# Kernel optimization log

Measured on AMD Instinct MI355X. Metric: run time of the kernel, lower is better.

## Reference

```python
import jax, jax.numpy as jnp
import numpy as np

KEEP_RATIO = 0.5
TEMPERATURE = 1.0
MIN_GATE = 0.0
EPS = 1e-06


def setup_inputs() -> dict:
    key = jax.random.key(0)
    k1, k2 = jax.random.split(key)
    B, C = 8192, 4096
    token = jax.random.normal(k1, (B, C), dtype=jnp.float32)
    proxy = jax.random.normal(k2, (B, C), dtype=jnp.float32)
    return {"token": token, "proxy": proxy}


def reference(token, proxy):
    tok = token  # [B, C]
    px = jax.lax.stop_gradient(proxy)  # detach_proxy=True
    score = jnp.abs(tok * px)  # [B, C]
    B, C = score.shape
    k = max(1, int(round(C * KEEP_RATIO)))
    # hard mask: top-k indices per row -> scatter 1.0
    _, topk_idx = jax.lax.top_k(score, k)  # [B, k]
    rows = jnp.arange(B)[:, None]
    hard_mask = jnp.zeros_like(score).at[rows, topk_idx].set(1.0)
    # per-row standardization (torch.std is unbiased -> ddof=1)
    mu = jnp.mean(score, axis=-1, keepdims=True)
    sigma = jnp.maximum(jnp.std(score, axis=-1, ddof=1, keepdims=True), EPS)
    z = (score - mu) / sigma / max(TEMPERATURE, EPS)
    soft_gate = jax.nn.sigmoid(z)
    if MIN_GATE > 0:
        soft_gate = soft_gate * (1.0 - MIN_GATE) + MIN_GATE
    gate = soft_gate * (1.0 - hard_mask) + hard_mask
    return tok * gate
```

## Files before the change

### kernel.cpp

```cpp
#include <hip/hip_runtime.h>
#include <math.h>

#define CLS   4096
#define KSEL  2048u
#define TPB   256

typedef float f32x4 __attribute__((ext_vector_type(4)));


template<int SHIFT, int NBITS, int BPL>
__device__ __forceinline__ void radix_small(const float sc[16], unsigned* hist,
        int lane, unsigned& prefix, unsigned& kr, unsigned& cnt_eq)
{
    const unsigned msk = (1u << NBITS) - 1u;
    #pragma unroll
    for (int i = 0; i < 16; ++i) {
        unsigned u = __float_as_uint(sc[i]);
        if ((u >> (SHIFT + NBITS)) == (prefix >> (SHIFT + NBITS)))
            atomicAdd(&hist[(u >> SHIFT) & msk], 1u);
    }
    __syncthreads();
    unsigned c[BPL];
    if constexpr (BPL == 4) {
        uint4 x = *(const uint4*)&hist[lane * 4];
        c[0] = x.x; c[1] = x.y; c[2] = x.z; c[3] = x.w;
    } else {
        c[0] = hist[lane];
    }
    unsigned sfx[BPL + 1]; sfx[BPL] = 0;
    #pragma unroll
    for (int j = BPL - 1; j >= 0; --j) sfx[j] = sfx[j + 1] + c[j];
    const unsigned tot = sfx[0];
    unsigned s = tot;
    #pragma unroll
    for (int off = 1; off < 64; off <<= 1) {
        unsigned t = __shfl_down(s, off);
        if (lane + off < 64) s += t;
    }
    const unsigned Sx = s - tot;
    const bool has = (Sx < kr) && (kr <= Sx + tot);
    unsigned bin = 0, below = 0, ceq = 0;
    if (has) {
        #pragma unroll
        for (int j = 0; j < BPL; ++j)
            if (Sx + sfx[j] >= kr && Sx + sfx[j + 1] < kr) {
                bin = (unsigned)(lane * BPL + j);
                below = Sx + sfx[j + 1];
                ceq = c[j];
            }
    }
    unsigned long long m = __ballot(has);
    int src = (int)__builtin_ctzll(m);
    bin = __shfl(bin, src); below = __shfl(below, src); ceq = __shfl(ceq, src);
    prefix |= bin << SHIFT;
    kr -= below;
    cnt_eq = ceq;
}

__global__ __launch_bounds__(TPB) void proxy_gate_kernel(
    const float* __restrict__ token,
    const float* __restrict__ proxy,
    float* __restrict__ out)
{
    __shared__ __align__(16) unsigned char lds[10304];
    unsigned* h0    = (unsigned*)(lds);
    unsigned* cand  = (unsigned*)(lds + 8192);
    unsigned* s_cnt = (unsigned*)(lds + 10240);
    unsigned* s_wt  = (unsigned*)(lds + 10244);
    unsigned* s_bc  = (unsigned*)(lds + 10260);
    float*    s_fr  = (float*)   (lds + 10272);
    unsigned char* s_flag = lds;
    unsigned*      s_suf  = (unsigned*)(lds + 4096);
    unsigned*      h1     = (unsigned*)(lds + 5120);
    unsigned*      h2     = (unsigned*)(lds + 6160);
    unsigned*      h3     = (unsigned*)(lds + 7200);

    const int tid  = threadIdx.x;
    const int lane = tid & 63;
    const int wv   = tid >> 6;
    const size_t base = (size_t)blockIdx.x * CLS;
    const float4* t4 = (const float4*)(token + base);
    const float4* p4 = (const float4*)(proxy + base);
    f32x4* o4 = (f32x4*)(out + base);

    float4 tv[4], pv[4];
    #pragma unroll
    for (int i = 0; i < 4; ++i) { tv[i] = t4[i*TPB + tid]; pv[i] = p4[i*TPB + tid]; }
    {
        uint4 z = make_uint4(0u, 0u, 0u, 0u);
        uint4* zp = (uint4*)lds;
        #pragma unroll
        for (int m = 0; m < 3; ++m) { int idx = m*TPB + tid; if (idx < 640) zp[idx] = z; }
        if (tid == 0) *s_cnt = 0u;
    }

    float sc[16];
    float sum = 0.f, sumsq = 0.f;
    #pragma unroll
    for (int i = 0; i < 4; ++i) {
        float a;
        a = fabsf(tv[i].x*pv[i].x); sc[i*4+0]=a; sum+=a; sumsq+=a*a;
        a = fabsf(tv[i].y*pv[i].y); sc[i*4+1]=a; sum+=a; sumsq+=a*a;
        a = fabsf(tv[i].z*pv[i].z); sc[i*4+2]=a; sum+=a; sumsq+=a*a;
        a = fabsf(tv[i].w*pv[i].w); sc[i*4+3]=a; sum+=a; sumsq+=a*a;
    }
    __syncthreads();

    #pragma unroll
    for (int i = 0; i < 16; ++i)
        atomicAdd(&h0[__float_as_uint(sc[i]) >> 20], 1u);
    #pragma unroll
    for (int off = 32; off > 0; off >>= 1) {
        sum   += __shfl_xor(sum, off);
        sumsq += __shfl_xor(sumsq, off);
    }
    if (lane == 0) { s_fr[wv] = sum; s_fr[4+wv] = sumsq; }
    __syncthreads();

    const float tot_s = s_fr[0]+s_fr[1]+s_fr[2]+s_fr[3];
    const float tot_q = s_fr[4]+s_fr[5]+s_fr[6]+s_fr[7];
    const float mu = tot_s * (1.0f/CLS);
    float var = (tot_q - tot_s*mu) * (1.0f/(CLS-1));
    var = fmaxf(var, 0.0f);
    const float inv_sigma = 1.0f / fmaxf(sqrtf(var), 1e-6f);

    unsigned kr = KSEL;
    {
        uint4 x0 = *(const uint4*)&h0[tid*8];
        uint4 x1 = *(const uint4*)&h0[tid*8 + 4];
        unsigned c[8] = { x0.x, x0.y, x0.z, x0.w, x1.x, x1.y, x1.z, x1.w };
        unsigned sfx[9]; sfx[8] = 0;
        #pragma unroll
        for (int j = 7; j >= 0; --j) sfx[j] = sfx[j+1] + c[j];
        const unsigned tot = sfx[0];
        unsigned s = tot;
        #pragma unroll
        for (int off = 1; off < 64; off <<= 1) {
            unsigned t = __shfl_down(s, off);
            if (lane + off < 64) s += t;
        }
        if (lane == 0) s_wt[wv] = s;
        __syncthreads();
        unsigned addhi = 0;
        #pragma unroll
        for (int w2 = 0; w2 < 4; ++w2) if (w2 > wv) addhi += s_wt[w2];
        const unsigned Sx = (s - tot) + addhi;
        if (Sx < kr && kr <= Sx + tot) {
            #pragma unroll
            for (int j = 0; j < 8; ++j)
                if (Sx + sfx[j] >= kr && Sx + sfx[j+1] < kr) {
                    s_bc[0] = (unsigned)(tid*8 + j);
                    s_bc[1] = Sx + sfx[j+1];
                    s_bc[2] = c[j];
                }
        }
        __syncthreads();
        kr -= s_bc[1];
    }
    const unsigned bin = s_bc[0];
    unsigned cnt_eq = s_bc[2];

    {
        unsigned cmask = 0, lc = 0;
        #pragma unroll
        for (int ii = 0; ii < 16; ++ii) {
            bool cnd = ((__float_as_uint(sc[ii]) >> 20) == bin);
            cmask |= ((unsigned)cnd) << ii;
            lc += (unsigned)cnd;
        }
        unsigned inc = lc;
        #pragma unroll
        for (int off = 1; off < 64; off <<= 1) {
            unsigned t = __shfl_up(inc, off);
            if (lane >= off) inc += t;
        }
        const unsigned wtot = __shfl(inc, 63);
        unsigned wbase = 0;
        if (lane == 0) wbase = atomicAdd(s_cnt, wtot);
        wbase = __shfl(wbase, 0);
        unsigned p = wbase + (inc - lc);
        #pragma unroll
        for (int ii = 0; ii < 16; ++ii) {
            if ((cmask >> ii) & 1u) {
                unsigned u = __float_as_uint(sc[ii]);
                unsigned idx = (unsigned)((ii >> 2)*1024 + tid*4 + (ii & 3));
                if (p < 512u) cand[p] = (u << 12) | (4095u - idx);
                ++p;
            }
        }
    }
    __syncthreads();
    const unsigned cnt = *s_cnt;
    const bool cand_mode = (cnt <= 512u);

    float thr = 0.f; bool tie_rare = false;
    if (cand_mode) {
        #pragma unroll
        for (int rpt = 0; rpt < 2; ++rpt) {
            const unsigned slot = (unsigned)tid + (unsigned)rpt*256u;
            if (slot < cnt) {
                const unsigned my = cand[slot];
                unsigned rank = 0;
                const uint4* c4 = (const uint4*)cand;
                const unsigned nq = (cnt + 3u) >> 2;
                for (unsigned q = 0; q < nq; ++q) {
                    uint4 v = c4[q];
                    rank += (unsigned)(v.x > my) + (unsigned)(v.y > my)
                          + (unsigned)(v.z > my) + (unsigned)(v.w > my);
                }
                if (rank == kr - 1u) s_bc[0] = my;
            }
        }
    } else {
        unsigned prefix = bin << 20;
        {
            unsigned* hz = (unsigned*)(lds + 5120);
            #pragma unroll
            for (int m = 0; m < 3; ++m) { int ix = m*TPB + tid; if (ix < 584) hz[ix] = 0u; }
        }
        __syncthreads();
        radix_small<12, 8, 4>(sc, h1, lane, prefix, kr, cnt_eq);
        radix_small< 4, 8, 4>(sc, h2, lane, prefix, kr, cnt_eq);
        radix_small< 0, 4, 1>(sc, h3, lane, prefix, kr, cnt_eq);
        thr = __uint_as_float(prefix);
        tie_rare = (cnt_eq != kr);
        if (tie_rare) {
            #pragma unroll
            for (int i = 0; i < 4; ++i)
                #pragma unroll
                for (int c2 = 0; c2 < 4; ++c2)
                    s_flag[i*1024 + tid*4 + c2] = (sc[i*4+c2] == thr) ? 1 : 0;
            __syncthreads();
            unsigned lc = 0;
            unsigned char mf[16];
            #pragma unroll
            for (int m = 0; m < 16; ++m) { mf[m] = s_flag[tid*16 + m]; lc += mf[m]; }
            s_suf[tid] = lc;
            __syncthreads();
            #pragma unroll
            for (int off = 1; off < 256; off <<= 1) {
                unsigned w = s_suf[tid] + ((tid >= off) ? s_suf[tid - off] : 0u);
                __syncthreads();
                s_suf[tid] = w;
                __syncthreads();
            }
            unsigned r2 = s_suf[tid] - lc;
            #pragma unroll
            for (int m = 0; m < 16; ++m) {
                if (mf[m]) { s_flag[tid*16 + m] = (r2 < kr) ? 2 : 0; ++r2; }
            }
        }
    }
    __syncthreads();
    const unsigned long long Kth64 =
        ((unsigned long long)bin << 32) | (unsigned long long)s_bc[0];

    const float A  = -inv_sigma * 1.44269504f;
    const float Bc = -mu * A;
    const unsigned rbase = 1023u - 4u*(unsigned)tid;
    #pragma unroll
    for (int i = 0; i < 4; ++i) {
        const float tkc[4] = { tv[i].x, tv[i].y, tv[i].z, tv[i].w };
        f32x4 rv;
        #pragma unroll
        for (int c2 = 0; c2 < 4; ++c2) {
            const float s = sc[i*4+c2];
            const float e2 = __builtin_amdgcn_exp2f(fmaf(s, A, Bc));
            const float soft = __builtin_amdgcn_rcpf(1.0f + e2);
            const unsigned u = __float_as_uint(s);
            bool hard;
            if (cand_mode) {
                const unsigned long long key =
                    ((unsigned long long)(u >> 20) << 32)
                    | (unsigned long long)((u << 12) | (rbase + (3u-(unsigned)i)*1024u - (unsigned)c2));
                hard = (key >= Kth64);
            } else if (tie_rare) {
                hard = (s > thr) || ((s == thr) && (s_flag[i*1024 + tid*4 + c2] == 2));
            } else {
                hard = (s >= thr);
            }
            rv[c2] = tkc[c2] * (hard ? 1.0f : soft);
        }
        __builtin_nontemporal_store(rv, &o4[i*TPB + tid]);
    }
}

extern "C" void kernel_launch(void* const* d_in, const int* in_sizes, int n_in,
                              void* d_out, int out_size, void* d_ws, size_t ws_size,
                              hipStream_t stream) {
    const float* token = (const float*)d_in[0];
    const float* proxy = (const float*)d_in[1];
    float* outp = (float*)d_out;
    const int B = in_sizes[0] / CLS;
    hipLaunchKernelGGL(proxy_gate_kernel, dim3(B), dim3(TPB), 0, stream,
                       token, proxy, outp);
}
```

Baseline: 66.44 us.

## Persistent blocks with async global-to-LDS prefetch of next row

Switches from one block per row to a persistent grid of up to 768 blocks, each looping over several rows. The next row's token and proxy data are prefetched into LDS with global_load_lds while the current row's top-k selection and gating run, so memory latency overlaps with compute. This costs about 43KB of LDS per block, which lowers occupancy, and adds per-row barriers and hand-written waitcnt tuning. The vmcnt(4) wait is fragile because it must account for the outstanding nontemporal stores.

```diff
diff --git a/kernel.cpp b/kernel.cpp
--- a/kernel.cpp
+++ b/kernel.cpp
@@ -4,9 +4,21 @@
 #define CLS   4096
 #define KSEL  2048u
 #define TPB   256
+#define NBLK  768
 
 typedef float f32x4 __attribute__((ext_vector_type(4)));
 
+
+#define BARRIER_LGKM() do { \
+    asm volatile("s_waitcnt lgkmcnt(0)" ::: "memory"); \
+    __builtin_amdgcn_s_barrier(); } while (0)
+
+__device__ __forceinline__ void gl_lds16(const float* g, void* l) {
+    __builtin_amdgcn_global_load_lds(
+        (const __attribute__((address_space(1))) unsigned int*)g,
+        (__attribute__((address_space(3))) unsigned int*)l,
+        16, 0, 0);
+}
 
 template<int SHIFT, int NBITS, int BPL>
 __device__ __forceinline__ void radix_small(const float sc[16], unsigned* hist,
@@ -60,228 +72,262 @@
 __global__ __launch_bounds__(TPB) void proxy_gate_kernel(
     const float* __restrict__ token,
     const float* __restrict__ proxy,
-    float* __restrict__ out)
+    float* __restrict__ out,
+    int nrows, int rpb)
 {
-    __shared__ __align__(16) unsigned char lds[10304];
-    unsigned* h0    = (unsigned*)(lds);
-    unsigned* cand  = (unsigned*)(lds + 8192);
-    unsigned* s_cnt = (unsigned*)(lds + 10240);
-    unsigned* s_wt  = (unsigned*)(lds + 10244);
-    unsigned* s_bc  = (unsigned*)(lds + 10260);
-    float*    s_fr  = (float*)   (lds + 10272);
-    unsigned char* s_flag = lds;
-    unsigned*      s_suf  = (unsigned*)(lds + 4096);
-    unsigned*      h1     = (unsigned*)(lds + 5120);
-    unsigned*      h2     = (unsigned*)(lds + 6160);
-    unsigned*      h3     = (unsigned*)(lds + 7200);
+    __shared__ __align__(16) unsigned char lds[43072];
+    unsigned* h0    = (unsigned*)(lds + 32768);
+    unsigned* cand  = (unsigned*)(lds + 40960);
+    unsigned* s_cnt = (unsigned*)(lds + 43008);
+    unsigned* s_wt  = (unsigned*)(lds + 43012);
+    unsigned* s_bc  = (unsigned*)(lds + 43028);
+    float*    s_fr  = (float*)   (lds + 43040);
+    unsigned char* s_flag = lds + 32768;
+    unsigned*      s_suf  = (unsigned*)(lds + 36864);
+    unsigned*      h1     = (unsigned*)(lds + 37888);
+    unsigned*      h2     = (unsigned*)(lds + 38928);
+    unsigned*      h3     = (unsigned*)(lds + 39968);
 
     const int tid  = threadIdx.x;
     const int lane = tid & 63;
     const int wv   = tid >> 6;
-    const size_t base = (size_t)blockIdx.x * CLS;
-    const float4* t4 = (const float4*)(token + base);
-    const float4* p4 = (const float4*)(proxy + base);
-    f32x4* o4 = (f32x4*)(out + base);
-
-    float4 tv[4], pv[4];
-    #pragma unroll
-    for (int i = 0; i < 4; ++i) { tv[i] = t4[i*TPB + tid]; pv[i] = p4[i*TPB + tid]; }
+    const int r0   = blockIdx.x * rpb;
+    if (r0 >= nrows) return;
+    const int r1   = (r0 + rpb < nrows) ? (r0 + rpb) : nrows;
+
     {
+        const float* tg = token + (size_t)r0 * CLS;
+        const float* pg = proxy + (size_t)r0 * CLS;
+        #pragma unroll
+        for (int i = 0; i < 4; ++i) {
+            gl_lds16(tg + i*1024 + tid*4, lds +         i*4096 + wv*1024);
+            gl_lds16(pg + i*1024 + tid*4, lds + 16384 + i*4096 + wv*1024);
+        }
         uint4 z = make_uint4(0u, 0u, 0u, 0u);
-        uint4* zp = (uint4*)lds;
+        uint4* zp = (uint4*)(lds + 32768);
         #pragma unroll
         for (int m = 0; m < 3; ++m) { int idx = m*TPB + tid; if (idx < 640) zp[idx] = z; }
         if (tid == 0) *s_cnt = 0u;
-    }
-
-    float sc[16];
-    float sum = 0.f, sumsq = 0.f;
-    #pragma unroll
-    for (int i = 0; i < 4; ++i) {
-        float a;
-        a = fabsf(tv[i].x*pv[i].x); sc[i*4+0]=a; sum+=a; sumsq+=a*a;
-        a = fabsf(tv[i].y*pv[i].y); sc[i*4+1]=a; sum+=a; sumsq+=a*a;
-        a = fabsf(tv[i].z*pv[i].z); sc[i*4+2]=a; sum+=a; sumsq+=a*a;
-        a = fabsf(tv[i].w*pv[i].w); sc[i*4+3]=a; sum+=a; sumsq+=a*a;
-    }
-    __syncthreads();
-
-    #pragma unroll
-    for (int i = 0; i < 16; ++i)
-        atomicAdd(&h0[__float_as_uint(sc[i]) >> 20], 1u);
-    #pragma unroll
-    for (int off = 32; off > 0; off >>= 1) {
-        sum   += __shfl_xor(sum, off);
-        sumsq += __shfl_xor(sumsq, off);
-    }
-    if (lane == 0) { s_fr[wv] = sum; s_fr[4+wv] = sumsq; }
-    __syncthreads();
-
-    const float tot_s = s_fr[0]+s_fr[1]+s_fr[2]+s_fr[3];
-    const float tot_q = s_fr[4]+s_fr[5]+s_fr[6]+s_fr[7];
-    const float mu = tot_s * (1.0f/CLS);
-    float var = (tot_q - tot_s*mu) * (1.0f/(CLS-1));
-    var = fmaxf(var, 0.0f);
-    const float inv_sigma = 1.0f / fmaxf(sqrtf(var), 1e-6f);
-
-    unsigned kr = KSEL;
-    {
-        uint4 x0 = *(const uint4*)&h0[tid*8];
-        uint4 x1 = *(const uint4*)&h0[tid*8 + 4];
-        unsigned c[8] = { x0.x, x0.y, x0.z, x0.w, x1.x, x1.y, x1.z, x1.w };
-        unsigned sfx[9]; sfx[8] = 0;
-        #pragma unroll
-        for (int j = 7; j >= 0; --j) sfx[j] = sfx[j+1] + c[j];
-        const unsigned tot = sfx[0];
-        unsigned s = tot;
-        #pragma unroll
-        for (int off = 1; off < 64; off <<= 1) {
-            unsigned t = __shfl_down(s, off);
-            if (lane + off < 64) s += t;
-        }
-        if (lane == 0) s_wt[wv] = s;
-        __syncthreads();
-        unsigned addhi = 0;
-        #pragma unroll
-        for (int w2 = 0; w2 < 4; ++w2) if (w2 > wv) addhi += s_wt[w2];
-        const unsigned Sx = (s - tot) + addhi;
-        if (Sx < kr && kr <= Sx + tot) {
-            #pragma unroll
-            for (int j = 0; j < 8; ++j)
-                if (Sx + sfx[j] >= kr && Sx + sfx[j+1] < kr) {
-                    s_bc[0] = (unsigned)(tid*8 + j);
-                    s_bc[1] = Sx + sfx[j+1];
-                    s_bc[2] = c[j];
-                }
-        }
-        __syncthreads();
-        kr -= s_bc[1];
-    }
-    const unsigned bin = s_bc[0];
-    unsigned cnt_eq = s_bc[2];
-
-    {
-        unsigned cmask = 0, lc = 0;
-        #pragma unroll
-        for (int ii = 0; ii < 16; ++ii) {
-            bool cnd = ((__float_as_uint(sc[ii]) >> 20) == bin);
-            cmask |= ((unsigned)cnd) << ii;
-            lc += (unsigned)cnd;
-        }
-        unsigned inc = lc;
-        #pragma unroll
-        for (int off = 1; off < 64; off <<= 1) {
-            unsigned t = __shfl_up(inc, off);
-            if (lane >= off) inc += t;
-        }
-        const unsigned wtot = __shfl(inc, 63);
-        unsigned wbase = 0;
-        if (lane == 0) wbase = atomicAdd(s_cnt, wtot);
-        wbase = __shfl(wbase, 0);
-        unsigned p = wbase + (inc - lc);
-        #pragma unroll
-        for (int ii = 0; ii < 16; ++ii) {
-            if ((cmask >> ii) & 1u) {
-                unsigned u = __float_as_uint(sc[ii]);
-                unsigned idx = (unsigned)((ii >> 2)*1024 + tid*4 + (ii & 3));
-                if (p < 512u) cand[p] = (u << 12) | (4095u - idx);
-                ++p;
-            }
-        }
-    }
-    __syncthreads();
-    const unsigned cnt = *s_cnt;
-    const bool cand_mode = (cnt <= 512u);
-
-    float thr = 0.f; bool tie_rare = false;
-    if (cand_mode) {
-        #pragma unroll
-        for (int rpt = 0; rpt < 2; ++rpt) {
-            const unsigned slot = (unsigned)tid + (unsigned)rpt*256u;
-            if (slot < cnt) {
-                const unsigned my = cand[slot];
-                unsigned rank = 0;
-                const uint4* c4 = (const uint4*)cand;
-                const unsigned nq = (cnt + 3u) >> 2;
-                for (unsigned q = 0; q < nq; ++q) {
-                    uint4 v = c4[q];
-                    rank += (unsigned)(v.x > my) + (unsigned)(v.y > my)
-                          + (unsigned)(v.z > my) + (unsigned)(v.w > my);
-                }
-                if (rank == kr - 1u) s_bc[0] = my;
-            }
-        }
-    } else {
-        unsigned prefix = bin << 20;
+        asm volatile("s_waitcnt vmcnt(0) lgkmcnt(0)" ::: "memory");
+        __builtin_amdgcn_s_barrier();
+    }
+
+    for (int row = r0; row < r1; ++row) {
+        float4 tv[4]; float sc[16];
+        float sum = 0.f, sumsq = 0.f;
+        #pragma unroll
+        for (int i = 0; i < 4; ++i) {
+            float4 t = *(const float4*)(lds +         i*4096 + tid*16);
+            float4 p = *(const float4*)(lds + 16384 + i*4096 + tid*16);
+            tv[i] = t;
+            float a;
+            a = fabsf(t.x*p.x); sc[i*4+0]=a; sum+=a; sumsq+=a*a;
+            a = fabsf(t.y*p.y); sc[i*4+1]=a; sum+=a; sumsq+=a*a;
+            a = fabsf(t.z*p.z); sc[i*4+2]=a; sum+=a; sumsq+=a*a;
+            a = fabsf(t.w*p.w); sc[i*4+3]=a; sum+=a; sumsq+=a*a;
+        }
+        BARRIER_LGKM();
+
+        if (row + 1 < r1) {
+            const float* tg = token + (size_t)(row+1) * CLS;
+            const float* pg = proxy + (size_t)(row+1) * CLS;
+            #pragma unroll
+            for (int i = 0; i < 4; ++i) {
+                gl_lds16(tg + i*1024 + tid*4, lds +         i*4096 + wv*1024);
+                gl_lds16(pg + i*1024 + tid*4, lds + 16384 + i*4096 + wv*1024);
+            }
+        }
+
+        #pragma unroll
+        for (int i = 0; i < 16; ++i)
+            atomicAdd(&h0[__float_as_uint(sc[i]) >> 20], 1u);
+        #pragma unroll
+        for (int off = 32; off > 0; off >>= 1) {
+            sum   += __shfl_xor(sum, off);
+            sumsq += __shfl_xor(sumsq, off);
+        }
+        if (lane == 0) { s_fr[wv] = sum; s_fr[4+wv] = sumsq; }
+        BARRIER_LGKM();
+
+        const float tot_s = s_fr[0]+s_fr[1]+s_fr[2]+s_fr[3];
+        const float tot_q = s_fr[4]+s_fr[5]+s_fr[6]+s_fr[7];
+        const float mu = tot_s * (1.0f/CLS);
+        float var = (tot_q - tot_s*mu) * (1.0f/(CLS-1));
+        var = fmaxf(var, 0.0f);
+        const float inv_sigma = 1.0f / fmaxf(sqrtf(var), 1e-6f);
+
+        unsigned kr = KSEL;
         {
-            unsigned* hz = (unsigned*)(lds + 5120);
-            #pragma unroll
-            for (int m = 0; m < 3; ++m) { int ix = m*TPB + tid; if (ix < 584) hz[ix] = 0u; }
-        }
-        __syncthreads();
-        radix_small<12, 8, 4>(sc, h1, lane, prefix, kr, cnt_eq);
-        radix_small< 4, 8, 4>(sc, h2, lane, prefix, kr, cnt_eq);
-        radix_small< 0, 4, 1>(sc, h3, lane, prefix, kr, cnt_eq);
-        thr = __uint_as_float(prefix);
-        tie_rare = (cnt_eq != kr);
-        if (tie_rare) {
-            #pragma unroll
-            for (int i = 0; i < 4; ++i)
-                #pragma unroll
-                for (int c2 = 0; c2 < 4; ++c2)
-                    s_flag[i*1024 + tid*4 + c2] = (sc[i*4+c2] == thr) ? 1 : 0;
+            uint4 x0 = *(const uint4*)&h0[tid*8];
+            uint4 x1 = *(const uint4*)&h0[tid*8 + 4];
+            unsigned c[8] = { x0.x, x0.y, x0.z, x0.w, x1.x, x1.y, x1.z, x1.w };
+            unsigned sfx[9]; sfx[8] = 0;
+            #pragma unroll
+            for (int j = 7; j >= 0; --j) sfx[j] = sfx[j+1] + c[j];
+            const unsigned tot = sfx[0];
+            unsigned s = tot;
+            #pragma unroll
+            for (int off = 1; off < 64; off <<= 1) {
+                unsigned t = __shfl_down(s, off);
+                if (lane + off < 64) s += t;
+            }
+            if (lane == 0) s_wt[wv] = s;
+            BARRIER_LGKM();
+            unsigned addhi = 0;
+            #pragma unroll
+            for (int w2 = 0; w2 < 4; ++w2) if (w2 > wv) addhi += s_wt[w2];
+            const unsigned Sx = (s - tot) + addhi;
+            if (Sx < kr && kr <= Sx + tot) {
+                #pragma unroll
+                for (int j = 0; j < 8; ++j)
+                    if (Sx + sfx[j] >= kr && Sx + sfx[j+1] < kr) {
+                        s_bc[0] = (unsigned)(tid*8 + j);
+                        s_bc[1] = Sx + sfx[j+1];
+                        s_bc[2] = c[j];
+                    }
+            }
+            BARRIER_LGKM();
+            kr -= s_bc[1];
+        }
+        const unsigned bin = s_bc[0];
+        unsigned cnt_eq = s_bc[2];
+
+        {
+            unsigned cmask = 0, lc = 0;
+            #pragma unroll
+            for (int ii = 0; ii < 16; ++ii) {
+                bool cnd = ((__float_as_uint(sc[ii]) >> 20) == bin);
+                cmask |= ((unsigned)cnd) << ii;
+                lc += (unsigned)cnd;
+            }
+            unsigned inc = lc;
+            #pragma unroll
+            for (int off = 1; off < 64; off <<= 1) {
+                unsigned t = __shfl_up(inc, off);
+                if (lane >= off) inc += t;
+            }
+            const unsigned wtot = __shfl(inc, 63);
+            unsigned wbase = 0;
+            if (lane == 0) wbase = atomicAdd(s_cnt, wtot);
+            wbase = __shfl(wbase, 0);
+            unsigned p = wbase + (inc - lc);
+            #pragma unroll
+            for (int ii = 0; ii < 16; ++ii) {
+                if ((cmask >> ii) & 1u) {
+                    unsigned u = __float_as_uint(sc[ii]);
+                    unsigned idx = (unsigned)((ii >> 2)*1024 + tid*4 + (ii & 3));
+                    if (p < 512u) cand[p] = (u << 12) | (4095u - idx);
+                    ++p;
+                }
+            }
+        }
+        BARRIER_LGKM();
+        const unsigned cnt = *s_cnt;
+        const bool cand_mode = (cnt <= 512u);
+
+        float thr = 0.f; bool tie_rare = false;
+        if (cand_mode) {
+            #pragma unroll
+            for (int rpt = 0; rpt < 2; ++rpt) {
+                const unsigned slot = (unsigned)tid + (unsigned)rpt*256u;
+                if (slot < cnt) {
+                    const unsigned my = cand[slot];
+                    unsigned rank = 0;
+                    const uint4* c4 = (const uint4*)cand;
+                    const unsigned nq = (cnt + 3u) >> 2;
+                    for (unsigned q = 0; q < nq; ++q) {
+                        uint4 v = c4[q];
+                        rank += (unsigned)(v.x > my) + (unsigned)(v.y > my)
+                              + (unsigned)(v.z > my) + (unsigned)(v.w > my);
+                    }
+                    if (rank == kr - 1u) s_bc[0] = my;
+                }
+            }
+        } else {
+            unsigned prefix = bin << 20;
+            {
+                unsigned* hz = (unsigned*)(lds + 37888);
+                #pragma unroll
+                for (int m = 0; m < 3; ++m) { int ix = m*TPB + tid; if (ix < 584) hz[ix] = 0u; }
+            }
             __syncthreads();
-            unsigned lc = 0;
-            unsigned char mf[16];
-            #pragma unroll
-            for (int m = 0; m < 16; ++m) { mf[m] = s_flag[tid*16 + m]; lc += mf[m]; }
-            s_suf[tid] = lc;
-            __syncthreads();
-            #pragma unroll
-            for (int off = 1; off < 256; off <<= 1) {
-                unsigned w = s_suf[tid] + ((tid >= off) ? s_suf[tid - off] : 0u);
+            radix_small<12, 8, 4>(sc, h1, lane, prefix, kr, cnt_eq);
+            radix_small< 4, 8, 4>(sc, h2, lane, prefix, kr, cnt_eq);
+            radix_small< 0, 4, 1>(sc, h3, lane, prefix, kr, cnt_eq);
+            thr = __uint_as_float(prefix);
+            tie_rare = (cnt_eq != kr);
+            if (tie_rare) {
+                #pragma unroll
+                for (int i = 0; i < 4; ++i)
+                    #pragma unroll
+                    for (int c2 = 0; c2 < 4; ++c2)
+                        s_flag[i*1024 + tid*4 + c2] = (sc[i*4+c2] == thr) ? 1 : 0;
                 __syncthreads();
-                s_suf[tid] = w;
+                unsigned lc = 0;
+                unsigned char mf[16];
+                #pragma unroll
+                for (int m = 0; m < 16; ++m) { mf[m] = s_flag[tid*16 + m]; lc += mf[m]; }
+                s_suf[tid] = lc;
                 __syncthreads();
-            }
-            unsigned r2 = s_suf[tid] - lc;
-            #pragma unroll
-            for (int m = 0; m < 16; ++m) {
-                if (mf[m]) { s_flag[tid*16 + m] = (r2 < kr) ? 2 : 0; ++r2; }
-            }
-        }
-    }
-    __syncthreads();
-    const unsigned long long Kth64 =
-        ((unsigned long long)bin << 32) | (unsigned long long)s_bc[0];
-
-    const float A  = -inv_sigma * 1.44269504f;
-    const float Bc = -mu * A;
-    const unsigned rbase = 1023u - 4u*(unsigned)tid;
-    #pragma unroll
-    for (int i = 0; i < 4; ++i) {
-        const float tkc[4] = { tv[i].x, tv[i].y, tv[i].z, tv[i].w };
-        f32x4 rv;
-        #pragma unroll
-        for (int c2 = 0; c2 < 4; ++c2) {
-            const float s = sc[i*4+c2];
-            const float e2 = __builtin_amdgcn_exp2f(fmaf(s, A, Bc));
-            const float soft = __builtin_amdgcn_rcpf(1.0f + e2);
-            const unsigned u = __float_as_uint(s);
-            bool hard;
-            if (cand_mode) {
-                const unsigned long long key =
-                    ((unsigned long long)(u >> 20) << 32)
-                    | (unsigned long long)((u << 12) | (rbase + (3u-(unsigned)i)*1024u - (unsigned)c2));
-                hard = (key >= Kth64);
-            } else if (tie_rare) {
-                hard = (s > thr) || ((s == thr) && (s_flag[i*1024 + tid*4 + c2] == 2));
-            } else {
-                hard = (s >= thr);
-            }
-            rv[c2] = tkc[c2] * (hard ? 1.0f : soft);
-        }
-        __builtin_nontemporal_store(rv, &o4[i*TPB + tid]);
+                #pragma unroll
+                for (int off = 1; off < 256; off <<= 1) {
+                    unsigned w = s_suf[tid] + ((tid >= off) ? s_suf[tid - off] : 0u);
+                    __syncthreads();
+                    s_suf[tid] = w;
+                    __syncthreads();
+                }
+                unsigned r2 = s_suf[tid] - lc;
+                #pragma unroll
+                for (int m = 0; m < 16; ++m) {
+                    if (mf[m]) { s_flag[tid*16 + m] = (r2 < kr) ? 2 : 0; ++r2; }
+                }
+            }
+        }
+        BARRIER_LGKM();
+        const unsigned long long Kth64 =
+            ((unsigned long long)bin << 32) | (unsigned long long)s_bc[0];
+
+        f32x4* o4 = (f32x4*)(out + (size_t)row * CLS);
+        const float A  = -inv_sigma * 1.44269504f;
+        const float Bc = -mu * A;
+        const unsigned rbase = 1023u - 4u*(unsigned)tid;
+        #pragma unroll
+        for (int i = 0; i < 4; ++i) {
+            const float tkc[4] = { tv[i].x, tv[i].y, tv[i].z, tv[i].w };
+            f32x4 rv;
+            #pragma unroll
+            for (int c2 = 0; c2 < 4; ++c2) {
+                const float s = sc[i*4+c2];
+                const float e2 = __builtin_amdgcn_exp2f(fmaf(s, A, Bc));
+                const float soft = __builtin_amdgcn_rcpf(1.0f + e2);
+                const unsigned u = __float_as_uint(s);
+                bool hard;
+                if (cand_mode) {
+                    const unsigned long long key =
+                        ((unsigned long long)(u >> 20) << 32)
+                        | (unsigned long long)((u << 12) | (rbase + (3u-(unsigned)i)*1024u - (unsigned)c2));
+                    hard = (key >= Kth64);
+                } else if (tie_rare) {
+                    hard = (s > thr) || ((s == thr) && (s_flag[i*1024 + tid*4 + c2] == 2));
+                } else {
+                    hard = (s >= thr);
+                }
+                rv[c2] = tkc[c2] * (hard ? 1.0f : soft);
+            }
+            __builtin_nontemporal_store(rv, &o4[i*TPB + tid]);
+        }
+
+        if (!cand_mode) { BARRIER_LGKM(); }
+
+        {
+            uint4 z = make_uint4(0u, 0u, 0u, 0u);
+            uint4* zp = (uint4*)(lds + 32768);
+            #pragma unroll
+            for (int m = 0; m < 3; ++m) { int idx = m*TPB + tid; if (idx < 640) zp[idx] = z; }
+            if (tid == 0) *s_cnt = 0u;
+        }
+        asm volatile("s_waitcnt vmcnt(4) lgkmcnt(0)" ::: "memory");
+        __builtin_amdgcn_s_barrier();
     }
 }
 
@@ -292,6 +338,8 @@
     const float* proxy = (const float*)d_in[1];
     float* outp = (float*)d_out;
     const int B = in_sizes[0] / CLS;
-    hipLaunchKernelGGL(proxy_gate_kernel, dim3(B), dim3(TPB), 0, stream,
-                       token, proxy, outp);
+    const int grid = (B < NBLK) ? B : NBLK;
+    const int rpb = (B + grid - 1) / grid;
+    hipLaunchKernelGGL(proxy_gate_kernel, dim3(grid), dim3(TPB), 0, stream,
+                       token, proxy, outp, B, rpb);
 }
```

Result: slower. 127.6 us (+92.0%).

## Make top-bin search and candidate ranking wave-redundant to drop block barriers

Applied to the files above, without the earlier changes.

The first-level histogram bin search now runs redundantly in every wavefront, using per-wave group sums, shuffles and a ballot, instead of a block scan that needed shared-memory exchange and two barriers. Candidate ranking in the small-candidate path is likewise done by each wave over all candidates, with the result broadcast by ballot and shuffle instead of written to shared memory, which removes a block-wide barrier. The final hard-mask test becomes a 32-bit comparison against the selected bin and key rather than a 64-bit key. The trade is redundant work per wave: every wave reads the whole histogram and ranks every candidate, up to 512, instead of splitting that work across 256 threads.

```diff
diff --git a/kernel.cpp b/kernel.cpp
--- a/kernel.cpp
+++ b/kernel.cpp
@@ -62,13 +62,11 @@
     const float* __restrict__ proxy,
     float* __restrict__ out)
 {
-    __shared__ __align__(16) unsigned char lds[10304];
+    __shared__ __align__(16) unsigned char lds[10288];
     unsigned* h0    = (unsigned*)(lds);
     unsigned* cand  = (unsigned*)(lds + 8192);
     unsigned* s_cnt = (unsigned*)(lds + 10240);
-    unsigned* s_wt  = (unsigned*)(lds + 10244);
-    unsigned* s_bc  = (unsigned*)(lds + 10260);
-    float*    s_fr  = (float*)   (lds + 10272);
+    float*    s_fr  = (float*)   (lds + 10244);
     unsigned char* s_flag = lds;
     unsigned*      s_suf  = (unsigned*)(lds + 4096);
     unsigned*      h1     = (unsigned*)(lds + 5120);
@@ -124,41 +122,52 @@
     var = fmaxf(var, 0.0f);
     const float inv_sigma = 1.0f / fmaxf(sqrtf(var), 1e-6f);
 
-    unsigned kr = KSEL;
+    unsigned kr = KSEL, bin = 0, cnt_eq = 0;
     {
-        uint4 x0 = *(const uint4*)&h0[tid*8];
-        uint4 x1 = *(const uint4*)&h0[tid*8 + 4];
-        unsigned c[8] = { x0.x, x0.y, x0.z, x0.w, x1.x, x1.y, x1.z, x1.w };
-        unsigned sfx[9]; sfx[8] = 0;
-        #pragma unroll
-        for (int j = 7; j >= 0; --j) sfx[j] = sfx[j+1] + c[j];
-        const unsigned tot = sfx[0];
-        unsigned s = tot;
-        #pragma unroll
-        for (int off = 1; off < 64; off <<= 1) {
-            unsigned t = __shfl_down(s, off);
-            if (lane + off < 64) s += t;
-        }
-        if (lane == 0) s_wt[wv] = s;
-        __syncthreads();
-        unsigned addhi = 0;
-        #pragma unroll
-        for (int w2 = 0; w2 < 4; ++w2) if (w2 > wv) addhi += s_wt[w2];
-        const unsigned Sx = (s - tot) + addhi;
-        if (Sx < kr && kr <= Sx + tot) {
-            #pragma unroll
-            for (int j = 0; j < 8; ++j)
-                if (Sx + sfx[j] >= kr && Sx + sfx[j+1] < kr) {
-                    s_bc[0] = (unsigned)(tid*8 + j);
-                    s_bc[1] = Sx + sfx[j+1];
-                    s_bc[2] = c[j];
+        const uint4* h4 = (const uint4*)h0;
+        unsigned g[8], S[8];
+        #pragma unroll
+        for (int w = 0; w < 8; ++w) {
+            uint4 q = h4[w*64 + lane];
+            g[w] = q.x + q.y + q.z + q.w;
+        }
+        #pragma unroll
+        for (int w = 0; w < 8; ++w) {
+            unsigned s = g[w];
+            #pragma unroll
+            for (int off = 1; off < 64; off <<= 1) {
+                unsigned t = __shfl_down(s, off);
+                if (lane + off < 64) s += t;
+            }
+            S[w] = s;
+        }
+        bool has = false;
+        unsigned fbin = 0, fbelow = 0, fceq = 0, up = 0;
+        #pragma unroll
+        for (int w = 7; w >= 0; --w) {
+            const unsigned Sx = up + S[w] - g[w];
+            if (Sx < kr && kr <= Sx + g[w]) {
+                uint4 q = h4[w*64 + lane];
+                const unsigned c[4] = { q.x, q.y, q.z, q.w };
+                unsigned r = Sx;
+                #pragma unroll
+                for (int j = 3; j >= 0; --j) {
+                    unsigned rn = r + c[j];
+                    if (r < kr && kr <= rn) {
+                        fbin = (unsigned)(w*256 + lane*4 + j);
+                        fbelow = r; fceq = c[j]; has = true;
+                    }
+                    r = rn;
                 }
-        }
-        __syncthreads();
-        kr -= s_bc[1];
-    }
-    const unsigned bin = s_bc[0];
-    unsigned cnt_eq = s_bc[2];
+            }
+            up += __shfl(S[w], 0);
+        }
+        unsigned long long m = __ballot(has);
+        int src = (int)__builtin_ctzll(m);
+        bin    = __shfl(fbin, src);
+        kr    -= __shfl(fbelow, src);
+        cnt_eq = __shfl(fceq, src);
+    }
 
     {
         unsigned cmask = 0, lc = 0;
@@ -193,24 +202,25 @@
     const unsigned cnt = *s_cnt;
     const bool cand_mode = (cnt <= 512u);
 
+    unsigned Kth = 0;
     float thr = 0.f; bool tie_rare = false;
     if (cand_mode) {
-        #pragma unroll
-        for (int rpt = 0; rpt < 2; ++rpt) {
-            const unsigned slot = (unsigned)tid + (unsigned)rpt*256u;
-            if (slot < cnt) {
-                const unsigned my = cand[slot];
-                unsigned rank = 0;
-                const uint4* c4 = (const uint4*)cand;
-                const unsigned nq = (cnt + 3u) >> 2;
-                for (unsigned q = 0; q < nq; ++q) {
-                    uint4 v = c4[q];
-                    rank += (unsigned)(v.x > my) + (unsigned)(v.y > my)
-                          + (unsigned)(v.z > my) + (unsigned)(v.w > my);
-                }
-                if (rank == kr - 1u) s_bc[0] = my;
-            }
-        }
+        unsigned myK = 0; bool found = false;
+        const uint4* c4 = (const uint4*)cand;
+        const unsigned nq = (cnt + 3u) >> 2;
+        for (unsigned slot = (unsigned)lane; slot < cnt; slot += 64u) {
+            const unsigned my = cand[slot];
+            unsigned rank = 0;
+            for (unsigned q = 0; q < nq; ++q) {
+                uint4 v = c4[q];
+                rank += (unsigned)(v.x > my) + (unsigned)(v.y > my)
+                      + (unsigned)(v.z > my) + (unsigned)(v.w > my);
+            }
+            if (rank == kr - 1u) { myK = my; found = true; }
+        }
+        unsigned long long m = __ballot(found);
+        int src = (int)__builtin_ctzll(m);
+        Kth = __shfl(myK, src);
     } else {
         unsigned prefix = bin << 20;
         {
@@ -250,14 +260,12 @@
                 if (mf[m]) { s_flag[tid*16 + m] = (r2 < kr) ? 2 : 0; ++r2; }
             }
         }
-    }
-    __syncthreads();
-    const unsigned long long Kth64 =
-        ((unsigned long long)bin << 32) | (unsigned long long)s_bc[0];
+        __syncthreads();
+    }
 
     const float A  = -inv_sigma * 1.44269504f;
     const float Bc = -mu * A;
-    const unsigned rbase = 1023u - 4u*(unsigned)tid;
+    const unsigned rbase = 4095u - 4u*(unsigned)tid;
     #pragma unroll
     for (int i = 0; i < 4; ++i) {
         const float tkc[4] = { tv[i].x, tv[i].y, tv[i].z, tv[i].w };
@@ -270,10 +278,9 @@
             const unsigned u = __float_as_uint(s);
             bool hard;
             if (cand_mode) {
-                const unsigned long long key =
-                    ((unsigned long long)(u >> 20) << 32)
-                    | (unsigned long long)((u << 12) | (rbase + (3u-(unsigned)i)*1024u - (unsigned)c2));
-                hard = (key >= Kth64);
+                const unsigned e = u >> 20;
+                const unsigned packed = (u << 12) | (rbase - 1024u*(unsigned)i - (unsigned)c2);
+                hard = (e > bin) || ((e == bin) && (packed >= Kth));
             } else if (tie_rare) {
                 hard = (s > thr) || ((s == thr) && (s_flag[i*1024 + tid*4 + c2] == 2));
             } else {
```

Measured after the change: 85.84 us. 29.2% more time.

## Split top-bin histogram into two copies and make candidate ranking wave-local

Applied to the files above, without the earlier changes.

The first-level 4096-bin LDS histogram is duplicated, with half the threads updating each copy, to reduce atomic contention; the copies are summed when the histogram is scanned. In candidate mode every wavefront now ranks all candidates redundantly and broadcasts the k-th key through ballot/shfl, instead of spreading the work across the block and publishing it through shared memory. This removes a block-wide barrier and the 64-bit key compare, but costs more LDS (affecting occupancy), extra zeroing work, and four times the ranking work per block.

```diff
diff --git a/kernel.cpp b/kernel.cpp
--- a/kernel.cpp
+++ b/kernel.cpp
@@ -62,13 +62,13 @@
     const float* __restrict__ proxy,
     float* __restrict__ out)
 {
-    __shared__ __align__(16) unsigned char lds[10304];
+    __shared__ __align__(16) unsigned char lds[18512];
     unsigned* h0    = (unsigned*)(lds);
-    unsigned* cand  = (unsigned*)(lds + 8192);
-    unsigned* s_cnt = (unsigned*)(lds + 10240);
-    unsigned* s_wt  = (unsigned*)(lds + 10244);
-    unsigned* s_bc  = (unsigned*)(lds + 10260);
-    float*    s_fr  = (float*)   (lds + 10272);
+    unsigned* cand  = (unsigned*)(lds + 16384);
+    unsigned* s_cnt = (unsigned*)(lds + 18432);
+    unsigned* s_wt  = (unsigned*)(lds + 18436);
+    unsigned* s_bc  = (unsigned*)(lds + 18452);
+    float*    s_fr  = (float*)   (lds + 18468);
     unsigned char* s_flag = lds;
     unsigned*      s_suf  = (unsigned*)(lds + 4096);
     unsigned*      h1     = (unsigned*)(lds + 5120);
@@ -90,7 +90,7 @@
         uint4 z = make_uint4(0u, 0u, 0u, 0u);
         uint4* zp = (uint4*)lds;
         #pragma unroll
-        for (int m = 0; m < 3; ++m) { int idx = m*TPB + tid; if (idx < 640) zp[idx] = z; }
+        for (int m = 0; m < 5; ++m) { int idx = m*TPB + tid; if (idx < 1152) zp[idx] = z; }
         if (tid == 0) *s_cnt = 0u;
     }
 
@@ -106,9 +106,12 @@
     }
     __syncthreads();
 
-    #pragma unroll
-    for (int i = 0; i < 16; ++i)
-        atomicAdd(&h0[__float_as_uint(sc[i]) >> 20], 1u);
+    {
+        unsigned* h0c = h0 + ((tid & 4) ? 2048 : 0);
+        #pragma unroll
+        for (int i = 0; i < 16; ++i)
+            atomicAdd(&h0c[__float_as_uint(sc[i]) >> 20], 1u);
+    }
     #pragma unroll
     for (int off = 32; off > 0; off >>= 1) {
         sum   += __shfl_xor(sum, off);
@@ -128,7 +131,10 @@
     {
         uint4 x0 = *(const uint4*)&h0[tid*8];
         uint4 x1 = *(const uint4*)&h0[tid*8 + 4];
-        unsigned c[8] = { x0.x, x0.y, x0.z, x0.w, x1.x, x1.y, x1.z, x1.w };
+        uint4 y0 = *(const uint4*)&h0[2048 + tid*8];
+        uint4 y1 = *(const uint4*)&h0[2048 + tid*8 + 4];
+        unsigned c[8] = { x0.x+y0.x, x0.y+y0.y, x0.z+y0.z, x0.w+y0.w,
+                          x1.x+y1.x, x1.y+y1.y, x1.z+y1.z, x1.w+y1.w };
         unsigned sfx[9]; sfx[8] = 0;
         #pragma unroll
         for (int j = 7; j >= 0; --j) sfx[j] = sfx[j+1] + c[j];
@@ -193,24 +199,25 @@
     const unsigned cnt = *s_cnt;
     const bool cand_mode = (cnt <= 512u);
 
+    unsigned Kth = 0;
     float thr = 0.f; bool tie_rare = false;
     if (cand_mode) {
-        #pragma unroll
-        for (int rpt = 0; rpt < 2; ++rpt) {
-            const unsigned slot = (unsigned)tid + (unsigned)rpt*256u;
-            if (slot < cnt) {
-                const unsigned my = cand[slot];
-                unsigned rank = 0;
-                const uint4* c4 = (const uint4*)cand;
-                const unsigned nq = (cnt + 3u) >> 2;
-                for (unsigned q = 0; q < nq; ++q) {
-                    uint4 v = c4[q];
-                    rank += (unsigned)(v.x > my) + (unsigned)(v.y > my)
-                          + (unsigned)(v.z > my) + (unsigned)(v.w > my);
-                }
-                if (rank == kr - 1u) s_bc[0] = my;
-            }
-        }
+        unsigned myK = 0; bool found = false;
+        const uint4* c4 = (const uint4*)cand;
+        const unsigned nq = (cnt + 3u) >> 2;
+        for (unsigned slot = (unsigned)lane; slot < cnt; slot += 64u) {
+            const unsigned my = cand[slot];
+            unsigned rank = 0;
+            for (unsigned q = 0; q < nq; ++q) {
+                uint4 v = c4[q];
+                rank += (unsigned)(v.x > my) + (unsigned)(v.y > my)
+                      + (unsigned)(v.z > my) + (unsigned)(v.w > my);
+            }
+            if (rank == kr - 1u) { myK = my; found = true; }
+        }
+        unsigned long long m = __ballot(found);
+        int src = (int)__builtin_ctzll(m);
+        Kth = __shfl(myK, src);
     } else {
         unsigned prefix = bin << 20;
         {
@@ -250,14 +257,12 @@
                 if (mf[m]) { s_flag[tid*16 + m] = (r2 < kr) ? 2 : 0; ++r2; }
             }
         }
-    }
-    __syncthreads();
-    const unsigned long long Kth64 =
-        ((unsigned long long)bin << 32) | (unsigned long long)s_bc[0];
+        __syncthreads();
+    }
 
     const float A  = -inv_sigma * 1.44269504f;
     const float Bc = -mu * A;
-    const unsigned rbase = 1023u - 4u*(unsigned)tid;
+    const unsigned rbase = 4095u - 4u*(unsigned)tid;
     #pragma unroll
     for (int i = 0; i < 4; ++i) {
         const float tkc[4] = { tv[i].x, tv[i].y, tv[i].z, tv[i].w };
@@ -270,10 +275,9 @@
             const unsigned u = __float_as_uint(s);
             bool hard;
             if (cand_mode) {
-                const unsigned long long key =
-                    ((unsigned long long)(u >> 20) << 32)
-                    | (unsigned long long)((u << 12) | (rbase + (3u-(unsigned)i)*1024u - (unsigned)c2));
-                hard = (key >= Kth64);
+                const unsigned e = u >> 20;
+                const unsigned packed = (u << 12) | (rbase - 1024u*(unsigned)i - (unsigned)c2);
+                hard = (e > bin) || ((e == bin) && (packed >= Kth));
             } else if (tie_rare) {
                 hard = (s > thr) || ((s == thr) && (s_flag[i*1024 + tid*4 + c2] == 2));
             } else {
```

Result: slower. 77.17 us (+16.2%).
